# Optimization experiments

Measured on AMD Instinct MI355X. Metric: run time of the kernel, lower is better.

## Reference

```python
import jax, jax.numpy as jnp
import numpy as np
import math

DIM, HEADS = 512, 8
D_K = DIM // HEADS

def setup_inputs() -> dict:
    key = jax.random.key(0)
    ks = jax.random.split(key, 6)
    B, LK, LQ = 16, 2048, 256
    s = 1.0 / math.sqrt(DIM)
    return {
        "L": jax.random.normal(ks[0], (B, LK, DIM), jnp.float32),
        "G": jax.random.normal(ks[1], (B, LQ, DIM), jnp.float32),
        "Wq": jax.random.normal(ks[2], (DIM, DIM), jnp.float32) * s,
        "bq": jnp.zeros((DIM,), jnp.float32),
        "Wo": jax.random.normal(ks[3], (DIM, DIM), jnp.float32) * s,
        "bo": jnp.zeros((DIM,), jnp.float32),
    }

def reference(L, G, Wq, bq, Wo, bo):
    B = G.shape[0]
    # Q projection from global tokens; K,V are raw local features split into heads
    q = (G @ Wq + bq).reshape(B, -1, HEADS, D_K)          # [B, Lq, H, d]
    k = L.reshape(B, -1, HEADS, D_K)                      # [B, Lk, H, d]
    v = k
    # double scaling as in source: / sqrt(d_k) * dim**-0.5
    scale = (D_K ** -0.5) * (DIM ** -0.5)
    dots = jnp.einsum("bqhd,bkhd->bhqk", q, k) * scale    # [B, H, Lq, Lk]
    attn = jax.nn.softmax(dots, axis=-1)
    x = jnp.einsum("bhqk,bkhd->bqhd", attn, v)            # [B, Lq, H, d]
    x = x.reshape(B, -1, HEADS * D_K)
    return x @ Wo + bo
```

## Files before the change

kernel.cpp:

```cpp
#include <hip/hip_runtime.h>

#define KSTR 72

typedef __attribute__((ext_vector_type(8))) short short8;
typedef __attribute__((ext_vector_type(4))) float f32x4;

#define EXP2F(x) __builtin_amdgcn_exp2f(x)

__device__ __forceinline__ unsigned short f2bf(float f) {
    union { float f; unsigned u; } v; v.f = f;
    unsigned r = v.u + 0x7fff + ((v.u >> 16) & 1);
    return (unsigned short)(r >> 16);
}
__device__ __forceinline__ unsigned pk2(float a, float b) {
    return (unsigned)f2bf(a) | ((unsigned)f2bf(b) << 16);
}

__global__ __launch_bounds__(256) void conv_W(const float* __restrict__ Wq,
                                              const float* __restrict__ Wo,
                                              unsigned short* __restrict__ WqF,
                                              unsigned short* __restrict__ WoF) {
    const float* W = blockIdx.y ? Wo : Wq;
    unsigned short* WF = blockIdx.y ? WoF : WqF;
    int g = blockIdx.x * 256 + threadIdx.x;
    int lane = g & 63, ntg = (g >> 6) & 31, kt = g >> 11;
    int c = lane & 15, quad = lane >> 4;
    const float* wp = W + (size_t)(32 * kt + 8 * quad) * 512 + 16 * ntg + c;
    float v[8];
    #pragma unroll
    for (int j = 0; j < 8; j++) v[j] = wp[(size_t)j * 512];
    uint4 u;
    u.x = pk2(v[0], v[1]); u.y = pk2(v[2], v[3]);
    u.z = pk2(v[4], v[5]); u.w = pk2(v[6], v[7]);
    *(uint4*)(WF + (size_t)g * 8) = u;
}

__global__ __launch_bounds__(256) void conv_L(const float* __restrict__ Lmat,
                                              unsigned short* __restrict__ KF,
                                              unsigned short* __restrict__ VF) {
    __shared__ unsigned short KFs[4096];
    __shared__ unsigned short VFs[4096];
    const int blk = blockIdx.x;
    const int t = blk & 31, h = (blk >> 5) & 7, b = blk >> 8;
    const int tid = threadIdx.x;
    const int key = tid & 63, wv = tid >> 6;

    const float* src = Lmat + ((size_t)(b * 2048 + 64 * t + key)) * 512 + 64 * h + 16 * wv;
    float4 a0 = *(const float4*)src;
    float4 a1 = *(const float4*)(src + 4);
    float4 a2 = *(const float4*)(src + 8);
    float4 a3 = *(const float4*)(src + 12);
    float vals[16] = {a0.x, a0.y, a0.z, a0.w, a1.x, a1.y, a1.z, a1.w,
                      a2.x, a2.y, a2.z, a2.w, a3.x, a3.y, a3.z, a3.w};
    #pragma unroll
    for (int i = 0; i < 16; i++) {
        int d = 16 * wv + i;
        unsigned short bv = f2bf(vals[i]);
        KFs[((((key >> 4) * 2 + (d >> 5)) * 64) + ((d >> 3) & 3) * 16 + (key & 15)) * 8 + (d & 7)] = bv;
        VFs[((((d >> 4) * 2 + (key >> 5)) * 64) + ((key >> 3) & 3) * 16 + (d & 15)) * 8 + (key & 7)] = bv;
    }
    __syncthreads();
    size_t gbase = (size_t)blk * 4096 + tid * 16;
    *(uint4*)(KF + gbase)     = *(const uint4*)&KFs[tid * 16];
    *(uint4*)(KF + gbase + 8) = *(const uint4*)&KFs[tid * 16 + 8];
    *(uint4*)(VF + gbase)     = *(const uint4*)&VFs[tid * 16];
    *(uint4*)(VF + gbase + 8) = *(const uint4*)&VFs[tid * 16 + 8];
}

template<bool A_BF16, bool OUT_BF16>
__global__ __launch_bounds__(256, 2) void gemm_direct(const void* __restrict__ Ap,
                                                      const unsigned short* __restrict__ WF,
                                                      const float* __restrict__ bias,
                                                      void* __restrict__ Cp,
                                                      float oscale) {
    const int tid = threadIdx.x;
    const int wv = tid >> 6, lane = tid & 63;
    const int c = lane & 15, quad = lane >> 4;
    const int m0 = blockIdx.x * 64, n0 = blockIdx.y * 64;
    const int row = m0 + 16 * wv + c;

    f32x4 acc[4];
    #pragma unroll
    for (int nt = 0; nt < 4; nt++) acc[nt] = (f32x4){0.f, 0.f, 0.f, 0.f};

    #pragma unroll
    for (int kk = 0; kk < 16; kk++) {
        short8 af;
        if (A_BF16) {
            af = *(const short8*)((const unsigned short*)Ap + (size_t)row * 512 + 32 * kk + 8 * quad);
        } else {
            const float* ap = (const float*)Ap + (size_t)row * 512 + 32 * kk + 8 * quad;
            float4 x0 = *(const float4*)ap;
            float4 x1 = *(const float4*)(ap + 4);
            af[0] = (short)f2bf(x0.x); af[1] = (short)f2bf(x0.y);
            af[2] = (short)f2bf(x0.z); af[3] = (short)f2bf(x0.w);
            af[4] = (short)f2bf(x1.x); af[5] = (short)f2bf(x1.y);
            af[6] = (short)f2bf(x1.z); af[7] = (short)f2bf(x1.w);
        }
        #pragma unroll
        for (int nt = 0; nt < 4; nt++) {
            short8 bf = *(const short8*)(WF +
                (((size_t)kk * 32 + (n0 >> 4) + nt) * 64 + lane) * 8);
            acc[nt] = __builtin_amdgcn_mfma_f32_16x16x32_bf16(af, bf, acc[nt], 0, 0, 0);
        }
    }

    #pragma unroll
    for (int nt = 0; nt < 4; nt++) {
        float bv = bias[n0 + 16 * nt + c];
        #pragma unroll
        for (int r = 0; r < 4; r++) {
            float v = (acc[nt][r] + bv) * oscale;
            size_t idx = (size_t)(m0 + 16 * wv + 4 * quad + r) * 512 + n0 + 16 * nt + c;
            if (OUT_BF16) ((unsigned short*)Cp)[idx] = f2bf(v);
            else          ((float*)Cp)[idx] = v;
        }
    }
}

__global__ __launch_bounds__(256, 2) void attn_frag(const unsigned short* __restrict__ Q,
                                                    const unsigned short* __restrict__ KF,
                                                    const unsigned short* __restrict__ VF,
                                                    unsigned short* __restrict__ X) {
    __shared__ unsigned short Pw[4][16 * KSTR];

    const int raw = blockIdx.x;
    const int h  = raw & 7;
    const int qt = (raw >> 3) & 3;
    const int b  = raw >> 5;
    const int tid = threadIdx.x;
    const int wv = tid >> 6, lane = tid & 63;
    const int c = lane & 15, quad = lane >> 4;

    short8 qa[2];
    {
        const unsigned short* qsrc =
            Q + ((size_t)(b * 256 + qt * 64 + 16 * wv + c)) * 512 + h * 64;
        qa[0] = *(const short8*)(qsrc + 8 * quad);
        qa[1] = *(const short8*)(qsrc + 32 + 8 * quad);
    }
    short8 ones;
    #pragma unroll
    for (int i = 0; i < 8; i++) ones[i] = (short)0x3F80;

    f32x4 oacc[4];
    #pragma unroll
    for (int dt = 0; dt < 4; dt++) oacc[dt] = (f32x4){0.f, 0.f, 0.f, 0.f};
    f32x4 lacc = (f32x4){0.f, 0.f, 0.f, 0.f};

    const int swc = (c >> 3) & 1;
    const int swr = (quad >> 1) & 1;

    const unsigned short* kf = KF + ((size_t)((b * 8 + h) * 32)) * 4096 + lane * 8;
    const unsigned short* vf = VF + ((size_t)((b * 8 + h) * 32)) * 4096 + lane * 8;

    short8 kc[8], vc[8], kn[8], vn[8];
    #pragma unroll
    for (int f = 0; f < 8; f++) {
        kc[f] = *(const short8*)(kf + f * 512);
        vc[f] = *(const short8*)(vf + f * 512);
    }

    auto compute = [&](short8* kb, short8* vb) {
        f32x4 sacc[4];
        #pragma unroll
        for (int nt = 0; nt < 4; nt++) sacc[nt] = (f32x4){0.f, 0.f, 0.f, 0.f};
        #pragma unroll
        for (int nt = 0; nt < 4; nt++)
            #pragma unroll
            for (int ks = 0; ks < 2; ks++)
                sacc[nt] = __builtin_amdgcn_mfma_f32_16x16x32_bf16(
                    qa[ks], kb[nt * 2 + ks], sacc[nt], 0, 0, 0);
        #pragma unroll
        for (int nt = 0; nt < 4; nt++)
            #pragma unroll
            for (int r = 0; r < 4; r++)
                Pw[wv][(4 * quad + r) * KSTR + ((16 * nt + c) ^ (8 * swr))] =
                    f2bf(EXP2F(sacc[nt][r]));
        short8 pa0 = *(const short8*)&Pw[wv][c * KSTR + (8 * (quad ^ swc))];
        short8 pa1 = *(const short8*)&Pw[wv][c * KSTR + 32 + (8 * (quad ^ swc))];
        #pragma unroll
        for (int dt = 0; dt < 4; dt++) {
            oacc[dt] = __builtin_amdgcn_mfma_f32_16x16x32_bf16(pa0, vb[dt * 2], oacc[dt], 0, 0, 0);
            oacc[dt] = __builtin_amdgcn_mfma_f32_16x16x32_bf16(pa1, vb[dt * 2 + 1], oacc[dt], 0, 0, 0);
        }
        lacc = __builtin_amdgcn_mfma_f32_16x16x32_bf16(pa0, ones, lacc, 0, 0, 0);
        lacc = __builtin_amdgcn_mfma_f32_16x16x32_bf16(pa1, ones, lacc, 0, 0, 0);
    };

    for (int t = 0; t < 32; t += 2) {
        {
            const unsigned short* k2 = kf + (size_t)(t + 1) * 4096;
            const unsigned short* v2 = vf + (size_t)(t + 1) * 4096;
            #pragma unroll
            for (int f = 0; f < 8; f++) {
                kn[f] = *(const short8*)(k2 + f * 512);
                vn[f] = *(const short8*)(v2 + f * 512);
            }
        }
        compute(kc, vc);
        if (t + 2 < 32) {
            const unsigned short* k2 = kf + (size_t)(t + 2) * 4096;
            const unsigned short* v2 = vf + (size_t)(t + 2) * 4096;
            #pragma unroll
            for (int f = 0; f < 8; f++) {
                kc[f] = *(const short8*)(k2 + f * 512);
                vc[f] = *(const short8*)(v2 + f * 512);
            }
        }
        compute(kn, vn);
    }

    #pragma unroll
    for (int r = 0; r < 4; r++) {
        float inv = 1.f / lacc[r];
        size_t row = (size_t)(b * 256 + qt * 64 + 16 * wv + 4 * quad + r);
        unsigned short* xp = X + row * 512 + h * 64;
        #pragma unroll
        for (int dt = 0; dt < 4; dt++)
            xp[16 * dt + c] = f2bf(oacc[dt][r] * inv);
    }
}

extern "C" void kernel_launch(void* const* d_in, const int* in_sizes, int n_in,
                              void* d_out, int out_size, void* d_ws, size_t ws_size,
                              hipStream_t stream) {
    const float* Lmat = (const float*)d_in[0];
    const float* G    = (const float*)d_in[1];
    const float* Wq   = (const float*)d_in[2];
    const float* bq   = (const float*)d_in[3];
    const float* Wo   = (const float*)d_in[4];
    const float* bo   = (const float*)d_in[5];
    float* out = (float*)d_out;

    const float SCe = 0.005524271728019903f * 1.4426950408889634f;
    dim3 gg(64, 8);

    unsigned short* Qws = (unsigned short*)d_ws;
    unsigned short* Xws = Qws + (size_t)2097152;
    unsigned short* WqF = Xws + (size_t)2097152;
    unsigned short* WoF = WqF + (size_t)262144;
    unsigned short* KF  = WoF + (size_t)262144;
    unsigned short* VF  = KF  + (size_t)16777216;

    conv_W<<<dim3(128, 2), 256, 0, stream>>>(Wq, Wo, WqF, WoF);
    conv_L<<<4096, 256, 0, stream>>>(Lmat, KF, VF);
    gemm_direct<false, true><<<gg, 256, 0, stream>>>(G, WqF, bq, Qws, SCe);
    attn_frag<<<512, 256, 0, stream>>>(Qws, KF, VF, Xws);
    gemm_direct<true, false><<<gg, 256, 0, stream>>>(Xws, WoF, bo, out, 1.0f);
}
```

Measured before the change: 180.7 us.

## Split attention key range across two wave groups and merge partial sums in LDS

```diff
diff --git a/kernel.cpp b/kernel.cpp
--- a/kernel.cpp
+++ b/kernel.cpp
@@ -118,11 +118,12 @@
     }
 }
 
-__global__ __launch_bounds__(256, 2) void attn_frag(const unsigned short* __restrict__ Q,
+__global__ __launch_bounds__(512, 4) void attn_frag(const unsigned short* __restrict__ Q,
                                                     const unsigned short* __restrict__ KF,
                                                     const unsigned short* __restrict__ VF,
                                                     unsigned short* __restrict__ X) {
-    __shared__ unsigned short Pw[4][16 * KSTR];
+    __shared__ unsigned short Pw[8][16 * KSTR];
+    __shared__ float Mrg[4][64][21];
 
     const int raw = blockIdx.x;
     const int h  = raw & 7;
@@ -130,12 +131,13 @@
     const int b  = raw >> 5;
     const int tid = threadIdx.x;
     const int wv = tid >> 6, lane = tid & 63;
+    const int wq = wv & 3, half = wv >> 2;
     const int c = lane & 15, quad = lane >> 4;
 
     short8 qa[2];
     {
         const unsigned short* qsrc =
-            Q + ((size_t)(b * 256 + qt * 64 + 16 * wv + c)) * 512 + h * 64;
+            Q + ((size_t)(b * 256 + qt * 64 + 16 * wq + c)) * 512 + h * 64;
         qa[0] = *(const short8*)(qsrc + 8 * quad);
         qa[1] = *(const short8*)(qsrc + 32 + 8 * quad);
     }
@@ -155,10 +157,11 @@
     const unsigned short* vf = VF + ((size_t)((b * 8 + h) * 32)) * 4096 + lane * 8;
 
     short8 kc[8], vc[8], kn[8], vn[8];
+    const int t0 = half * 16;
     #pragma unroll
     for (int f = 0; f < 8; f++) {
-        kc[f] = *(const short8*)(kf + f * 512);
-        vc[f] = *(const short8*)(vf + f * 512);
+        kc[f] = *(const short8*)(kf + (size_t)t0 * 4096 + f * 512);
+        vc[f] = *(const short8*)(vf + (size_t)t0 * 4096 + f * 512);
     }
 
     auto compute = [&](short8* kb, short8* vb) {
@@ -188,7 +191,7 @@
         lacc = __builtin_amdgcn_mfma_f32_16x16x32_bf16(pa1, ones, lacc, 0, 0, 0);
     };
 
-    for (int t = 0; t < 32; t += 2) {
+    for (int t = t0; t < t0 + 16; t += 2) {
         {
             const unsigned short* k2 = kf + (size_t)(t + 1) * 4096;
             const unsigned short* v2 = vf + (size_t)(t + 1) * 4096;
@@ -199,7 +202,7 @@
             }
         }
         compute(kc, vc);
-        if (t + 2 < 32) {
+        if (t + 2 < t0 + 16) {
             const unsigned short* k2 = kf + (size_t)(t + 2) * 4096;
             const unsigned short* v2 = vf + (size_t)(t + 2) * 4096;
             #pragma unroll
@@ -211,14 +214,32 @@
         compute(kn, vn);
     }
 
-    #pragma unroll
-    for (int r = 0; r < 4; r++) {
-        float inv = 1.f / lacc[r];
-        size_t row = (size_t)(b * 256 + qt * 64 + 16 * wv + 4 * quad + r);
-        unsigned short* xp = X + row * 512 + h * 64;
+    if (half) {
         #pragma unroll
         for (int dt = 0; dt < 4; dt++)
-            xp[16 * dt + c] = f2bf(oacc[dt][r] * inv);
+            #pragma unroll
+            for (int r = 0; r < 4; r++) Mrg[wq][lane][4 * dt + r] = oacc[dt][r];
+        #pragma unroll
+        for (int r = 0; r < 4; r++) Mrg[wq][lane][16 + r] = lacc[r];
+    }
+    __syncthreads();
+    if (!half) {
+        #pragma unroll
+        for (int dt = 0; dt < 4; dt++)
+            #pragma unroll
+            for (int r = 0; r < 4; r++) oacc[dt][r] += Mrg[wq][lane][4 * dt + r];
+        #pragma unroll
+        for (int r = 0; r < 4; r++) lacc[r] += Mrg[wq][lane][16 + r];
+
+        #pragma unroll
+        for (int r = 0; r < 4; r++) {
+            float inv = 1.f / lacc[r];
+            size_t row = (size_t)(b * 256 + qt * 64 + 16 * wq + 4 * quad + r);
+            unsigned short* xp = X + row * 512 + h * 64;
+            #pragma unroll
+            for (int dt = 0; dt < 4; dt++)
+                xp[16 * dt + c] = f2bf(oacc[dt][r] * inv);
+        }
     }
 }
 
@@ -246,6 +267,6 @@
     conv_W<<<dim3(128, 2), 256, 0, stream>>>(Wq, Wo, WqF, WoF);
     conv_L<<<4096, 256, 0, stream>>>(Lmat, KF, VF);
     gemm_direct<false, true><<<gg, 256, 0, stream>>>(G, WqF, bq, Qws, SCe);
-    attn_frag<<<512, 256, 0, stream>>>(Qws, KF, VF, Xws);
+    attn_frag<<<512, 512, 0, stream>>>(Qws, KF, VF, Xws);
     gemm_direct<true, false><<<gg, 256, 0, stream>>>(Xws, WoF, bo, out, 1.0f);
 }
```

New measurement: 280.9 us. +55.4%, slower.

## Split key tiles across waves in attention and reduce partial outputs via LDS

Applied to the files above, without the earlier changes.

```diff
diff --git a/kernel.cpp b/kernel.cpp
--- a/kernel.cpp
+++ b/kernel.cpp
@@ -122,7 +122,9 @@
                                                     const unsigned short* __restrict__ KF,
                                                     const unsigned short* __restrict__ VF,
                                                     unsigned short* __restrict__ X) {
-    __shared__ unsigned short Pw[4][16 * KSTR];
+    __shared__ __align__(16) char shm_raw[4 * 64 * 68 * 4];
+    unsigned short (*Pw)[4][16 * KSTR] = (unsigned short (*)[4][16 * KSTR])shm_raw;
+    float (*Mrg)[64][68] = (float (*)[64][68])shm_raw;
 
     const int raw = blockIdx.x;
     const int h  = raw & 7;
@@ -132,21 +134,27 @@
     const int wv = tid >> 6, lane = tid & 63;
     const int c = lane & 15, quad = lane >> 4;
 
-    short8 qa[2];
-    {
+    short8 qa[4][2];
+    #pragma unroll
+    for (int g = 0; g < 4; g++) {
         const unsigned short* qsrc =
-            Q + ((size_t)(b * 256 + qt * 64 + 16 * wv + c)) * 512 + h * 64;
-        qa[0] = *(const short8*)(qsrc + 8 * quad);
-        qa[1] = *(const short8*)(qsrc + 32 + 8 * quad);
-    }
+            Q + ((size_t)(b * 256 + qt * 64 + 16 * g + c)) * 512 + h * 64;
+        qa[g][0] = *(const short8*)(qsrc + 8 * quad);
+        qa[g][1] = *(const short8*)(qsrc + 32 + 8 * quad);
+    }
+
     short8 ones;
     #pragma unroll
     for (int i = 0; i < 8; i++) ones[i] = (short)0x3F80;
 
-    f32x4 oacc[4];
-    #pragma unroll
-    for (int dt = 0; dt < 4; dt++) oacc[dt] = (f32x4){0.f, 0.f, 0.f, 0.f};
-    f32x4 lacc = (f32x4){0.f, 0.f, 0.f, 0.f};
+    f32x4 oacc[4][4];
+    #pragma unroll
+    for (int g = 0; g < 4; g++)
+        #pragma unroll
+        for (int dt = 0; dt < 4; dt++) oacc[g][dt] = (f32x4){0.f, 0.f, 0.f, 0.f};
+    f32x4 lacc[4];
+    #pragma unroll
+    for (int g = 0; g < 4; g++) lacc[g] = (f32x4){0.f, 0.f, 0.f, 0.f};
 
     const int swc = (c >> 3) & 1;
     const int swr = (quad >> 1) & 1;
@@ -154,71 +162,85 @@
     const unsigned short* kf = KF + ((size_t)((b * 8 + h) * 32)) * 4096 + lane * 8;
     const unsigned short* vf = VF + ((size_t)((b * 8 + h) * 32)) * 4096 + lane * 8;
 
-    short8 kc[8], vc[8], kn[8], vn[8];
-    #pragma unroll
-    for (int f = 0; f < 8; f++) {
-        kc[f] = *(const short8*)(kf + f * 512);
-        vc[f] = *(const short8*)(vf + f * 512);
-    }
-
-    auto compute = [&](short8* kb, short8* vb) {
-        f32x4 sacc[4];
-        #pragma unroll
-        for (int nt = 0; nt < 4; nt++) sacc[nt] = (f32x4){0.f, 0.f, 0.f, 0.f};
-        #pragma unroll
-        for (int nt = 0; nt < 4; nt++)
-            #pragma unroll
-            for (int ks = 0; ks < 2; ks++)
-                sacc[nt] = __builtin_amdgcn_mfma_f32_16x16x32_bf16(
-                    qa[ks], kb[nt * 2 + ks], sacc[nt], 0, 0, 0);
-        #pragma unroll
-        for (int nt = 0; nt < 4; nt++)
+    for (int i = 0; i < 8; i++) {
+        const int T = wv + 4 * i;
+        const unsigned short* kt = kf + (size_t)T * 4096;
+        const unsigned short* vt = vf + (size_t)T * 4096;
+        short8 kbuf[8], vbuf[8];
+        #pragma unroll
+        for (int f = 0; f < 8; f++) kbuf[f] = *(const short8*)(kt + f * 512);
+        #pragma unroll
+        for (int f = 0; f < 8; f++) vbuf[f] = *(const short8*)(vt + f * 512);
+
+        #pragma unroll
+        for (int g = 0; g < 4; g++) {
+            f32x4 sacc[4];
+            #pragma unroll
+            for (int nt = 0; nt < 4; nt++) sacc[nt] = (f32x4){0.f, 0.f, 0.f, 0.f};
+            __builtin_amdgcn_s_setprio(1);
+            #pragma unroll
+            for (int nt = 0; nt < 4; nt++)
+                #pragma unroll
+                for (int ks = 0; ks < 2; ks++)
+                    sacc[nt] = __builtin_amdgcn_mfma_f32_16x16x32_bf16(
+                        qa[g][ks], kbuf[nt * 2 + ks], sacc[nt], 0, 0, 0);
+            __builtin_amdgcn_s_setprio(0);
+            #pragma unroll
+            for (int nt = 0; nt < 4; nt++)
+                #pragma unroll
+                for (int r = 0; r < 4; r++)
+                    Pw[wv][g][(4 * quad + r) * KSTR + ((16 * nt + c) ^ (8 * swr))] =
+                        f2bf(EXP2F(sacc[nt][r]));
+        }
+        #pragma unroll
+        for (int g = 0; g < 4; g++) {
+            short8 pa0 = *(const short8*)&Pw[wv][g][c * KSTR + 8 * (quad ^ swc)];
+            short8 pa1 = *(const short8*)&Pw[wv][g][c * KSTR + 32 + 8 * (quad ^ swc)];
+            __builtin_amdgcn_s_setprio(1);
+            #pragma unroll
+            for (int dt = 0; dt < 4; dt++) {
+                oacc[g][dt] = __builtin_amdgcn_mfma_f32_16x16x32_bf16(pa0, vbuf[dt * 2], oacc[g][dt], 0, 0, 0);
+                oacc[g][dt] = __builtin_amdgcn_mfma_f32_16x16x32_bf16(pa1, vbuf[dt * 2 + 1], oacc[g][dt], 0, 0, 0);
+            }
+            lacc[g] = __builtin_amdgcn_mfma_f32_16x16x32_bf16(pa0, ones, lacc[g], 0, 0, 0);
+            lacc[g] = __builtin_amdgcn_mfma_f32_16x16x32_bf16(pa1, ones, lacc[g], 0, 0, 0);
+            __builtin_amdgcn_s_setprio(0);
+        }
+    }
+
+    __syncthreads();
+    #pragma unroll
+    for (int g = 0; g < 4; g++) {
+        #pragma unroll
+        for (int dt = 0; dt < 4; dt++)
             #pragma unroll
             for (int r = 0; r < 4; r++)
-                Pw[wv][(4 * quad + r) * KSTR + ((16 * nt + c) ^ (8 * swr))] =
-                    f2bf(EXP2F(sacc[nt][r]));
-        short8 pa0 = *(const short8*)&Pw[wv][c * KSTR + (8 * (quad ^ swc))];
-        short8 pa1 = *(const short8*)&Pw[wv][c * KSTR + 32 + (8 * (quad ^ swc))];
-        #pragma unroll
-        for (int dt = 0; dt < 4; dt++) {
-            oacc[dt] = __builtin_amdgcn_mfma_f32_16x16x32_bf16(pa0, vb[dt * 2], oacc[dt], 0, 0, 0);
-            oacc[dt] = __builtin_amdgcn_mfma_f32_16x16x32_bf16(pa1, vb[dt * 2 + 1], oacc[dt], 0, 0, 0);
-        }
-        lacc = __builtin_amdgcn_mfma_f32_16x16x32_bf16(pa0, ones, lacc, 0, 0, 0);
-        lacc = __builtin_amdgcn_mfma_f32_16x16x32_bf16(pa1, ones, lacc, 0, 0, 0);
-    };
-
-    for (int t = 0; t < 32; t += 2) {
-        {
-            const unsigned short* k2 = kf + (size_t)(t + 1) * 4096;
-            const unsigned short* v2 = vf + (size_t)(t + 1) * 4096;
-            #pragma unroll
-            for (int f = 0; f < 8; f++) {
-                kn[f] = *(const short8*)(k2 + f * 512);
-                vn[f] = *(const short8*)(v2 + f * 512);
-            }
-        }
-        compute(kc, vc);
-        if (t + 2 < 32) {
-            const unsigned short* k2 = kf + (size_t)(t + 2) * 4096;
-            const unsigned short* v2 = vf + (size_t)(t + 2) * 4096;
-            #pragma unroll
-            for (int f = 0; f < 8; f++) {
-                kc[f] = *(const short8*)(k2 + f * 512);
-                vc[f] = *(const short8*)(v2 + f * 512);
-            }
-        }
-        compute(kn, vn);
-    }
-
-    #pragma unroll
-    for (int r = 0; r < 4; r++) {
-        float inv = 1.f / lacc[r];
-        size_t row = (size_t)(b * 256 + qt * 64 + 16 * wv + 4 * quad + r);
-        unsigned short* xp = X + row * 512 + h * 64;
-        #pragma unroll
-        for (int dt = 0; dt < 4; dt++)
-            xp[16 * dt + c] = f2bf(oacc[dt][r] * inv);
+                Mrg[wv][g * 16 + 4 * quad + r][16 * dt + c] = oacc[g][dt][r];
+        #pragma unroll
+        for (int r = 0; r < 4; r++)
+            Mrg[wv][g * 16 + 4 * quad + r][64] = lacc[g][r];
+    }
+    __syncthreads();
+    {
+        const int row = 16 * wv + c;
+        float sum[16];
+        #pragma unroll
+        for (int j = 0; j < 16; j++) sum[j] = 0.f;
+        float lsum = 0.f;
+        #pragma unroll
+        for (int ws = 0; ws < 4; ws++) {
+            #pragma unroll
+            for (int j = 0; j < 16; j++) sum[j] += Mrg[ws][row][16 * quad + j];
+            lsum += Mrg[ws][row][64];
+        }
+        float inv = 1.f / lsum;
+        unsigned short us[16];
+        #pragma unroll
+        for (int j = 0; j < 16; j++) us[j] = f2bf(sum[j] * inv);
+        unsigned short* xp =
+            X + ((size_t)(b * 256 + qt * 64 + row)) * 512 + h * 64 + 16 * quad;
+        *(uint4*)(xp)     = *(uint4*)&us[0];
+        *(uint4*)(xp + 8) = *(uint4*)&us[8];
     }
 }
 
```

Measured after the change: 170.1 us. -5.9%, faster.
